# Kernel tuning notes

Hardware: AMD Instinct MI355X
Metric: run time of the kernel (lower is better)

Reference implementation:

```python
import math
import jax, jax.numpy as jnp
import numpy as np

D_MODEL = 512
N_HEADS = 8
D_K = D_MODEL // N_HEADS
LN_EPS = 1e-5


def _rel_pos_encoding(length: int, d: int) -> jnp.ndarray:
    """Sinusoidal encodings for positions 0..length-1, shape (length, d)."""
    pos = jnp.arange(length, dtype=jnp.float32)[:, None]            # (L,1)
    div = jnp.exp(jnp.arange(0, d, 2, dtype=jnp.float32) * (-(math.log(10000.0) / d)))  # (d/2,)
    ang = pos * div[None, :]                                         # (L,d/2)
    # interleave sin (even cols) and cos (odd cols)
    return jnp.stack([jnp.sin(ang), jnp.cos(ang)], axis=-1).reshape(length, d)


def setup_inputs() -> dict:
    key = jax.random.key(0)
    ks = jax.random.split(key, 6)
    B, T = 4, 2048
    s = 1.0 / math.sqrt(D_MODEL)
    return {
        "x":    jax.random.normal(ks[0], (B, T, D_MODEL), dtype=jnp.float32),
        "ln_g": jnp.ones((D_MODEL,), jnp.float32),
        "ln_b": jnp.zeros((D_MODEL,), jnp.float32),
        "wq":   jax.random.normal(ks[1], (D_MODEL, D_MODEL), jnp.float32) * s,
        "bq":   jnp.zeros((D_MODEL,), jnp.float32),
        "wk":   jax.random.normal(ks[2], (D_MODEL, D_MODEL), jnp.float32) * s,
        "bk":   jnp.zeros((D_MODEL,), jnp.float32),
        "wv":   jax.random.normal(ks[3], (D_MODEL, D_MODEL), jnp.float32) * s,
        "bv":   jnp.zeros((D_MODEL,), jnp.float32),
        "wo":   jax.random.normal(ks[4], (D_MODEL, D_MODEL), jnp.float32) * s,
        "bo":   jnp.zeros((D_MODEL,), jnp.float32),
    }


def reference(x, ln_g, ln_b, wq, bq, wk, bk, wv, bv, wo, bo):
    B, T, D = x.shape
    # pre-norm LayerNorm
    mu = jnp.mean(x, axis=-1, keepdims=True)
    var = jnp.mean(jnp.square(x - mu), axis=-1, keepdims=True)
    normed = (x - mu) * jax.lax.rsqrt(var + LN_EPS) * ln_g + ln_b

    def split_heads(y):  # (B,T,D) -> (B,H,T,dk)
        return y.reshape(B, T, N_HEADS, D_K).transpose(0, 2, 1, 3)

    Q = split_heads(normed @ wq.T + bq)
    K = split_heads(normed @ wk.T + bk)
    V = split_heads(normed @ wv.T + bv)

    pe = _rel_pos_encoding(T, D_K)            # (T, dk)
    K = K + pe[None, None, :, :]              # additive relative PE on K

    scale = 1.0 / math.sqrt(D_K)
    scores = jnp.einsum('bhtd,bhsd->bhts', Q, K) * scale   # (B,H,T,T)
    attn = jax.nn.softmax(scores, axis=-1)
    context = jnp.einsum('bhts,bhsd->bhtd', attn, V)        # (B,H,T,dk)
    context = context.transpose(0, 2, 1, 3).reshape(B, T, D)
    return context @ wo.T + bo
```

## Files before the change

### kernel.cpp

```cpp
#include <hip/hip_runtime.h>
#include <hip/hip_bf16.h>
#include <math.h>

#define D_MODEL 512
#define N_HEADS 8
#define D_K     64
#define T_SEQ   2048
#define B_SZ    4
#define M_ROWS  (B_SZ * T_SEQ)

typedef __bf16 bf16;
typedef __bf16 bf16x4 __attribute__((ext_vector_type(4)));
typedef __bf16 bf16x8 __attribute__((ext_vector_type(8)));
typedef float  floatx4 __attribute__((ext_vector_type(4)));

__device__ __forceinline__ int SWZ(int row, int col) {
  return row * 64 + ((((col >> 3) ^ (row & 7)) << 3) | (col & 7));
}

__device__ __forceinline__ float pe_fast(int t, int d) {
  int i2 = d & ~1;
  float div = __expf((float)i2 * (-0.1439115683f));
  float ang = (float)t * div;
  return (d & 1) ? __cosf(ang) : __sinf(ang);
}

__global__ __launch_bounds__(256) void prep(
    const float* __restrict__ x, const float* __restrict__ g,
    const float* __restrict__ b, bf16* __restrict__ out,
    const float* __restrict__ wq, const float* __restrict__ wk,
    const float* __restrict__ wv, const float* __restrict__ wo,
    bf16* __restrict__ wdst) {
  int bid = blockIdx.x;
  int tid = threadIdx.x;
  if (bid >= M_ROWS / 4) {
    int gid = (bid - M_ROWS / 4) * 256 + tid;
    int e0  = gid * 4;
    int mat = e0 >> 18;
    int loc = e0 & 262143;
    const float* src = (mat == 0) ? wq : (mat == 1) ? wk : (mat == 2) ? wv : wo;
    float4 v = *(const float4*)(src + loc);
    bf16x4 pk;
    pk[0] = (bf16)v.x; pk[1] = (bf16)v.y; pk[2] = (bf16)v.z; pk[3] = (bf16)v.w;
    *(bf16x4*)(wdst + e0) = pk;
    return;
  }
  int wave = tid >> 6, lane = tid & 63;
  int row  = bid * 4 + wave;
  const float* xr = x + (size_t)row * D_MODEL + lane * 8;
  float4 a = *(const float4*)(xr);
  float4 c = *(const float4*)(xr + 4);
  float s  = a.x + a.y + a.z + a.w + c.x + c.y + c.z + c.w;
  float ss = a.x * a.x + a.y * a.y + a.z * a.z + a.w * a.w +
             c.x * c.x + c.y * c.y + c.z * c.z + c.w * c.w;
#pragma unroll
  for (int off = 1; off < 64; off <<= 1) {
    s  += __shfl_xor(s,  off, 64);
    ss += __shfl_xor(ss, off, 64);
  }
  float mu  = s * (1.0f / D_MODEL);
  float var = ss * (1.0f / D_MODEL) - mu * mu;
  float rs  = rsqrtf(var + 1e-5f);
  float4 g0 = *(const float4*)(g + lane * 8);
  float4 g1 = *(const float4*)(g + lane * 8 + 4);
  float4 b0 = *(const float4*)(b + lane * 8);
  float4 b1 = *(const float4*)(b + lane * 8 + 4);
  bf16x8 o8;
  o8[0] = (bf16)((a.x - mu) * rs * g0.x + b0.x);
  o8[1] = (bf16)((a.y - mu) * rs * g0.y + b0.y);
  o8[2] = (bf16)((a.z - mu) * rs * g0.z + b0.z);
  o8[3] = (bf16)((a.w - mu) * rs * g0.w + b0.w);
  o8[4] = (bf16)((c.x - mu) * rs * g1.x + b1.x);
  o8[5] = (bf16)((c.y - mu) * rs * g1.y + b1.y);
  o8[6] = (bf16)((c.z - mu) * rs * g1.z + b1.z);
  o8[7] = (bf16)((c.w - mu) * rs * g1.w + b1.w);
  *(bf16x8*)(out + (size_t)row * D_MODEL + lane * 8) = o8;
}

__global__ __launch_bounds__(256, 3) void gemm_qkv(
    const bf16* __restrict__ A, const bf16* __restrict__ wqkv,
    const float* __restrict__ bq, const float* __restrict__ bk, const float* __restrict__ bv,
    bf16* __restrict__ Qo, bf16* __restrict__ Ko, bf16* __restrict__ VTo) {
  __shared__ bf16 sW[16384];
  __shared__ bf16 ep[4][1536];

  int tid = threadIdx.x;
  int w = tid >> 6, lane = tid & 63;
  int lm = lane & 15, quad = lane >> 4;
  int mat  = blockIdx.y >> 3;
  int h    = blockIdx.y & 7;
  int nloc = h * 64;
  const bf16* Wp = wqkv + (size_t)mat * 262144;

  int mbase = blockIdx.x * 128 + w * 32;
  const bf16* ap = A + (size_t)(mbase + lm) * D_MODEL + quad * 8;

  floatx4 acc[2][4];
#pragma unroll
  for (int mi = 0; mi < 2; mi++)
#pragma unroll
    for (int nt = 0; nt < 4; nt++) acc[mi][nt] = floatx4{0.f, 0.f, 0.f, 0.f};

  int srow = tid >> 2;
  int scc  = (tid & 3) * 16;

#pragma unroll 1
  for (int kp = 0; kp < 2; kp++) {
    if (kp) __syncthreads();
#pragma unroll
    for (int kc = 0; kc < 4; kc++) {
      const bf16* src = Wp + (size_t)(nloc + srow) * D_MODEL + kp * 256 + kc * 64 + scc;
      bf16x8 w0 = *(const bf16x8*)src;
      bf16x8 w1 = *(const bf16x8*)(src + 8);
      *(bf16x8*)&sW[kc * 4096 + SWZ(srow, scc)]     = w0;
      *(bf16x8*)&sW[kc * 4096 + SWZ(srow, scc + 8)] = w1;
    }
    __syncthreads();

    bf16x8 af[2][8];
#pragma unroll
    for (int mi = 0; mi < 2; mi++)
#pragma unroll
      for (int ks = 0; ks < 8; ks++)
        af[mi][ks] = *(const bf16x8*)(ap + mi * 16 * D_MODEL + kp * 256 + ks * 32);

#pragma unroll
    for (int ks = 0; ks < 8; ks++) {
#pragma unroll
      for (int nt = 0; nt < 4; nt++) {
        bf16x8 bfr = *(const bf16x8*)
            &sW[(ks >> 1) * 4096 + SWZ(nt * 16 + lm, (ks & 1) * 32 + quad * 8)];
        acc[0][nt] = __builtin_amdgcn_mfma_f32_16x16x32_bf16(af[0][ks], bfr, acc[0][nt], 0, 0, 0);
        acc[1][nt] = __builtin_amdgcn_mfma_f32_16x16x32_bf16(af[1][ks], bfr, acc[1][nt], 0, 0, 0);
      }
    }
  }

  int bb = mbase >> 11, t0w = mbase & (T_SEQ - 1);
  size_t bhoff = (size_t)(bb * N_HEADS + h) * (T_SEQ * D_K);
  bf16* myep = ep[w];

  if (mat == 2) {
#pragma unroll
    for (int nt = 0; nt < 4; nt++) {
      float bvv = bv[nloc + nt * 16 + lm];
#pragma unroll
      for (int mi = 0; mi < 2; mi++) {
        bf16x4 pk;
#pragma unroll
        for (int rr = 0; rr < 4; rr++) pk[rr] = (bf16)(acc[mi][nt][rr] + bvv);
        *(bf16x4*)&myep[lm * 40 + mi * 16 + quad * 4] = pk;
      }
      int dl = lane >> 2, toff = (lane & 3) * 8;
      bf16x8 v = *(const bf16x8*)&myep[dl * 40 + toff];
      *(bf16x8*)(VTo + bhoff + (size_t)(nt * 16 + dl) * T_SEQ + t0w + toff) = v;
    }
  } else {
    bf16* dst = (mat == 0) ? Qo : Ko;
    const float* bias = (mat == 0) ? bq : bk;
#pragma unroll
    for (int c = 0; c < 2; c++) {
#pragma unroll
      for (int nt = 0; nt < 4; nt++) {
        int d = nt * 16 + lm;
        float bval = bias[nloc + d];
#pragma unroll
        for (int rr = 0; rr < 4; rr++) {
          float v = acc[c][nt][rr] + bval;
          if (mat == 1) v += pe_fast(t0w + c * 16 + quad * 4 + rr, d);
          else          v *= 0.125f;
          myep[(quad * 4 + rr) * 72 + d] = (bf16)v;
        }
      }
#pragma unroll
      for (int rd = 0; rd < 2; rd++) {
        int row = rd * 8 + (lane >> 3);
        bf16x8 v = *(const bf16x8*)&myep[row * 72 + (lane & 7) * 8];
        *(bf16x8*)(dst + bhoff + (size_t)(t0w + c * 16 + row) * D_K + (lane & 7) * 8) = v;
      }
    }
  }
}

__global__ __launch_bounds__(256, 3) void gemm_out(const bf16* __restrict__ A,
                                                   const bf16* __restrict__ W,
                                                   const float* __restrict__ bias,
                                                   float* __restrict__ out) {
  __shared__ bf16 sW[16384];
  int tid = threadIdx.x;
  int w = tid >> 6, lane = tid & 63;
  int lm = lane & 15, quad = lane >> 4;
  int n0 = blockIdx.y * 64;

  int mbase = blockIdx.x * 128 + w * 32;
  const bf16* ap = A + (size_t)(mbase + lm) * D_MODEL + quad * 8;

  floatx4 acc[2][4];
#pragma unroll
  for (int mi = 0; mi < 2; mi++)
#pragma unroll
    for (int nt = 0; nt < 4; nt++) acc[mi][nt] = floatx4{0.f, 0.f, 0.f, 0.f};

  int srow = tid >> 2;
  int scc  = (tid & 3) * 16;

#pragma unroll 1
  for (int kp = 0; kp < 2; kp++) {
    if (kp) __syncthreads();
#pragma unroll
    for (int kc = 0; kc < 4; kc++) {
      const bf16* src = W + (size_t)(n0 + srow) * D_MODEL + kp * 256 + kc * 64 + scc;
      bf16x8 w0 = *(const bf16x8*)src;
      bf16x8 w1 = *(const bf16x8*)(src + 8);
      *(bf16x8*)&sW[kc * 4096 + SWZ(srow, scc)]     = w0;
      *(bf16x8*)&sW[kc * 4096 + SWZ(srow, scc + 8)] = w1;
    }
    __syncthreads();

    bf16x8 af[2][8];
#pragma unroll
    for (int mi = 0; mi < 2; mi++)
#pragma unroll
      for (int ks = 0; ks < 8; ks++)
        af[mi][ks] = *(const bf16x8*)(ap + mi * 16 * D_MODEL + kp * 256 + ks * 32);

#pragma unroll
    for (int ks = 0; ks < 8; ks++) {
#pragma unroll
      for (int nt = 0; nt < 4; nt++) {
        bf16x8 bfr = *(const bf16x8*)
            &sW[(ks >> 1) * 4096 + SWZ(nt * 16 + lm, (ks & 1) * 32 + quad * 8)];
        acc[0][nt] = __builtin_amdgcn_mfma_f32_16x16x32_bf16(af[0][ks], bfr, acc[0][nt], 0, 0, 0);
        acc[1][nt] = __builtin_amdgcn_mfma_f32_16x16x32_bf16(af[1][ks], bfr, acc[1][nt], 0, 0, 0);
      }
    }
  }

#pragma unroll
  for (int nt = 0; nt < 4; nt++) {
    int n = n0 + nt * 16 + lm;
    float bval = bias[n];
#pragma unroll
    for (int mi = 0; mi < 2; mi++)
#pragma unroll
      for (int rr = 0; rr < 4; rr++) {
        int m = mbase + mi * 16 + quad * 4 + rr;
        out[(size_t)m * D_MODEL + n] = acc[mi][nt][rr] + bval;
      }
  }
}

__global__ __launch_bounds__(512, 4) void flash_mfma(const bf16* __restrict__ Q,
                                                     const bf16* __restrict__ K,
                                                     const bf16* __restrict__ VT,
                                                     bf16* __restrict__ ctx) {
  __shared__ __align__(16) char smem[65536];
  bf16* sK  = (bf16*)smem;
  bf16* sVT = (bf16*)(smem + 16384);
  bf16* sP  = (bf16*)(smem + 32768);

  int tid  = threadIdx.x;
  int wave = tid >> 6, lane = tid & 63;
  int lm = lane & 15, quad = lane >> 4;
  int qg = wave & 3, kg = wave >> 2;
  int bh = blockIdx.y;
  int q0 = blockIdx.x * 128 + qg * 32;

  const bf16* Qb  = Q  + (size_t)bh * T_SEQ * D_K;
  const bf16* Kb  = K  + (size_t)bh * T_SEQ * D_K;
  const bf16* VTb = VT + (size_t)bh * T_SEQ * D_K;

  bf16x8 qf[2][2];
#pragma unroll
  for (int qt = 0; qt < 2; qt++)
#pragma unroll
    for (int kb = 0; kb < 2; kb++)
      qf[qt][kb] = *(const bf16x8*)(Qb + (size_t)(q0 + qt * 16 + lm) * D_K + kb * 32 + quad * 8);

  floatx4 o[2][4];
#pragma unroll
  for (int qt = 0; qt < 2; qt++)
#pragma unroll
    for (int nt = 0; nt < 4; nt++) o[qt][nt] = floatx4{0.f, 0.f, 0.f, 0.f};
  float l_i[2] = {0.f, 0.f};

  int srow = tid >> 3;
  int scol = (tid & 7) * 8;
  const bf16* kp0 = Kb  + (size_t)srow * D_K + scol;
  const bf16* vp0 = VTb + (size_t)srow * T_SEQ + scol;

  bf16x8 rk[2], rv[2];
  rk[0] = *(const bf16x8*)(kp0);
  rk[1] = *(const bf16x8*)(kp0 + 4096);
  rv[0] = *(const bf16x8*)(vp0);
  rv[1] = *(const bf16x8*)(vp0 + 64);

  bf16* myK = sK  + kg * 4096;
  bf16* myV = sVT + kg * 4096;
  bf16* myP = sP  + wave * 2048;

  for (int r = 0; r < T_SEQ / 64; r += 2) {
    __syncthreads();
    *(bf16x8*)&sK [SWZ(srow, scol)]         = rk[0];
    *(bf16x8*)&sK [4096 + SWZ(srow, scol)]  = rk[1];
    *(bf16x8*)&sVT[SWZ(srow, scol)]         = rv[0];
    *(bf16x8*)&sVT[4096 + SWZ(srow, scol)]  = rv[1];
    if (r + 2 < T_SEQ / 64) {
      rk[0] = *(const bf16x8*)(kp0 + (r + 2) * 4096);
      rk[1] = *(const bf16x8*)(kp0 + (r + 3) * 4096);
      rv[0] = *(const bf16x8*)(vp0 + (r + 2) * 64);
      rv[1] = *(const bf16x8*)(vp0 + (r + 3) * 64);
    }
    __syncthreads();

#pragma unroll
    for (int nt = 0; nt < 4; nt++) {
      floatx4 s0 = floatx4{0.f, 0.f, 0.f, 0.f};
      floatx4 s1 = floatx4{0.f, 0.f, 0.f, 0.f};
#pragma unroll
      for (int kb = 0; kb < 2; kb++) {
        bf16x8 kf = *(const bf16x8*)&myK[SWZ(nt * 16 + lm, kb * 32 + quad * 8)];
        s0 = __builtin_amdgcn_mfma_f32_16x16x32_bf16(kf, qf[0][kb], s0, 0, 0, 0);
        s1 = __builtin_amdgcn_mfma_f32_16x16x32_bf16(kf, qf[1][kb], s1, 0, 0, 0);
      }
      bf16x4 pk0, pk1;
#pragma unroll
      for (int rr = 0; rr < 4; rr++) {
        float p0 = __expf(s0[rr] - 8.0f);
        float p1 = __expf(s1[rr] - 8.0f);
        l_i[0] += p0; l_i[1] += p1;
        pk0[rr] = (bf16)p0; pk1[rr] = (bf16)p1;
      }
      *(bf16x4*)&myP[SWZ(lm,      nt * 16 + quad * 4)] = pk0;
      *(bf16x4*)&myP[SWZ(16 + lm, nt * 16 + quad * 4)] = pk1;
    }

#pragma unroll
    for (int kb = 0; kb < 2; kb++) {
      bf16x8 pf0 = *(const bf16x8*)&myP[SWZ(lm, kb * 32 + quad * 8)];
      bf16x8 pf1 = *(const bf16x8*)&myP[SWZ(16 + lm, kb * 32 + quad * 8)];
#pragma unroll
      for (int nt = 0; nt < 4; nt++) {
        bf16x8 vt = *(const bf16x8*)&myV[SWZ(nt * 16 + lm, kb * 32 + quad * 8)];
        o[0][nt] = __builtin_amdgcn_mfma_f32_16x16x32_bf16(pf0, vt, o[0][nt], 0, 0, 0);
        o[1][nt] = __builtin_amdgcn_mfma_f32_16x16x32_bf16(pf1, vt, o[1][nt], 0, 0, 0);
      }
    }
  }

#pragma unroll
  for (int qt = 0; qt < 2; qt++) {
    l_i[qt] += __shfl_xor(l_i[qt], 16, 64);
    l_i[qt] += __shfl_xor(l_i[qt], 32, 64);
  }

  __syncthreads();
  float* scO = (float*)smem;
  float* scL = (float*)(smem + 32768);
  if (kg == 1) {
#pragma unroll
    for (int qt = 0; qt < 2; qt++)
#pragma unroll
      for (int nt = 0; nt < 4; nt++)
        *(floatx4*)&scO[(qg * 512 + (qt * 4 + nt) * 64 + lane) * 4] = o[qt][nt];
    scL[qg * 128 + lane]      = l_i[0];
    scL[qg * 128 + 64 + lane] = l_i[1];
  }
  __syncthreads();
  if (kg == 0) {
#pragma unroll
    for (int qt = 0; qt < 2; qt++)
#pragma unroll
      for (int nt = 0; nt < 4; nt++) {
        floatx4 t = *(const floatx4*)&scO[(qg * 512 + (qt * 4 + nt) * 64 + lane) * 4];
        o[qt][nt] += t;
      }
    l_i[0] += scL[qg * 128 + lane];
    l_i[1] += scL[qg * 128 + 64 + lane];

    int b_ = bh >> 3, h = bh & 7;
#pragma unroll
    for (int qt = 0; qt < 2; qt++) {
#pragma unroll
      for (int rr = 0; rr < 4; rr++) {
        int qq = quad * 4 + rr;
        float linv = 1.f / __shfl(l_i[qt], qq, 64);
        int t = q0 + qt * 16 + qq;
        bf16* op = ctx + ((size_t)(b_ * T_SEQ + t)) * D_MODEL + h * D_K;
#pragma unroll
        for (int nt = 0; nt < 4; nt++)
          op[nt * 16 + lm] = (bf16)(o[qt][nt][rr] * linv);
      }
    }
  }
}

extern "C" void kernel_launch(void* const* d_in, const int* in_sizes, int n_in,
                              void* d_out, int out_size, void* d_ws, size_t ws_size,
                              hipStream_t stream) {
  const float* x    = (const float*)d_in[0];
  const float* ln_g = (const float*)d_in[1];
  const float* ln_b = (const float*)d_in[2];
  const float* wq   = (const float*)d_in[3];
  const float* bq   = (const float*)d_in[4];
  const float* wk   = (const float*)d_in[5];
  const float* bk   = (const float*)d_in[6];
  const float* wv   = (const float*)d_in[7];
  const float* bv   = (const float*)d_in[8];
  const float* wo   = (const float*)d_in[9];
  const float* bo   = (const float*)d_in[10];
  float* out = (float*)d_out;

  char* ws = (char*)d_ws;
  const size_t MB8 = (size_t)M_ROWS * D_MODEL * sizeof(bf16);
  bf16* normed = (bf16*)(ws);
  bf16* Qb     = (bf16*)(ws + MB8);
  bf16* Kb     = (bf16*)(ws + 2 * MB8);
  bf16* VTb    = (bf16*)(ws + 3 * MB8);
  bf16* w4     = (bf16*)(ws + 4 * MB8);
  bf16* ctx    = normed;

  prep<<<M_ROWS / 4 + 1024, 256, 0, stream>>>(x, ln_g, ln_b, normed,
                                              wq, wk, wv, wo, w4);
  gemm_qkv<<<dim3(64, 24), 256, 0, stream>>>(
      normed, w4, bq, bk, bv, Qb, Kb, VTb);
  flash_mfma<<<dim3(T_SEQ / 128, B_SZ * N_HEADS), 512, 0, stream>>>(Qb, Kb, VTb, ctx);
  gemm_out<<<dim3(64, 8), 256, 0, stream>>>(
      ctx, w4 + 3 * (size_t)D_MODEL * D_MODEL, bo, out);
}
```

Before: 177.1 us.

## Switch flash attention to 32x32x16 MFMA with register-resident P via permlane swap

Rewrites the attention inner loop to use 32x32x16 bf16 MFMA tiles instead of 16x16x32. The probability matrix is no longer staged through LDS: it is converted with v_cvt_pk_bf16_f32 and rearranged across lane halves with v_permlane32_swap, so it can be fed directly as the A operand of the PV MFMA. This removes the LDS round trip for P, shrinks shared memory from 64KB to 34KB (possibly raising occupancy), and changes the final reduction and output layout to match. The register-level lane shuffle depends on an exact layout match between the MFMA output and input formats, which is a correctness risk.

After: 178.5 us. Within noise of the previous version (+0.8%).

```diff
diff --git a/kernel.cpp b/kernel.cpp
--- a/kernel.cpp
+++ b/kernel.cpp
@@ -13,9 +13,20 @@
 typedef __bf16 bf16x4 __attribute__((ext_vector_type(4)));
 typedef __bf16 bf16x8 __attribute__((ext_vector_type(8)));
 typedef float  floatx4 __attribute__((ext_vector_type(4)));
+typedef float  floatx16 __attribute__((ext_vector_type(16)));
 
 __device__ __forceinline__ int SWZ(int row, int col) {
   return row * 64 + ((((col >> 3) ^ (row & 7)) << 3) | (col & 7));
+}
+
+__device__ __forceinline__ unsigned cvtpk(float a, float b) {
+  unsigned r;
+  asm volatile("v_cvt_pk_bf16_f32 %0, %1, %2" : "=v"(r) : "v"(a), "v"(b));
+  return r;
+}
+
+__device__ __forceinline__ void plswap(unsigned& a, unsigned& b) {
+  asm volatile("v_permlane32_swap_b32 %0, %1" : "+v"(a), "+v"(b));
 }
 
 __device__ __forceinline__ float pe_fast(int t, int d) {
@@ -254,14 +265,13 @@
                                                      const bf16* __restrict__ K,
                                                      const bf16* __restrict__ VT,
                                                      bf16* __restrict__ ctx) {
-  __shared__ __align__(16) char smem[65536];
+  __shared__ __align__(16) char smem[34816];
   bf16* sK  = (bf16*)smem;
   bf16* sVT = (bf16*)(smem + 16384);
-  bf16* sP  = (bf16*)(smem + 32768);
 
   int tid  = threadIdx.x;
   int wave = tid >> 6, lane = tid & 63;
-  int lm = lane & 15, quad = lane >> 4;
+  int lq = lane & 31, hi = lane >> 5;
   int qg = wave & 3, kg = wave >> 2;
   int bh = blockIdx.y;
   int q0 = blockIdx.x * 128 + qg * 32;
@@ -270,19 +280,15 @@
   const bf16* Kb  = K  + (size_t)bh * T_SEQ * D_K;
   const bf16* VTb = VT + (size_t)bh * T_SEQ * D_K;
 
-  bf16x8 qf[2][2];
-#pragma unroll
-  for (int qt = 0; qt < 2; qt++)
-#pragma unroll
-    for (int kb = 0; kb < 2; kb++)
-      qf[qt][kb] = *(const bf16x8*)(Qb + (size_t)(q0 + qt * 16 + lm) * D_K + kb * 32 + quad * 8);
-
-  floatx4 o[2][4];
-#pragma unroll
-  for (int qt = 0; qt < 2; qt++)
-#pragma unroll
-    for (int nt = 0; nt < 4; nt++) o[qt][nt] = floatx4{0.f, 0.f, 0.f, 0.f};
-  float l_i[2] = {0.f, 0.f};
+  bf16x8 qf[4];
+#pragma unroll
+  for (int c = 0; c < 4; c++)
+    qf[c] = *(const bf16x8*)(Qb + (size_t)(q0 + lq) * D_K + c * 16 + hi * 8);
+
+  floatx16 o0 = {0.f}, o1 = {0.f};
+#pragma unroll
+  for (int r = 0; r < 16; r++) { o0[r] = 0.f; o1[r] = 0.f; }
+  float l_i = 0.f;
 
   int srow = tid >> 3;
   int scol = (tid & 7) * 8;
@@ -297,7 +303,6 @@
 
   bf16* myK = sK  + kg * 4096;
   bf16* myV = sVT + kg * 4096;
-  bf16* myP = sP  + wave * 2048;
 
   for (int r = 0; r < T_SEQ / 64; r += 2) {
     __syncthreads();
@@ -314,83 +319,71 @@
     __syncthreads();
 
 #pragma unroll
-    for (int nt = 0; nt < 4; nt++) {
-      floatx4 s0 = floatx4{0.f, 0.f, 0.f, 0.f};
-      floatx4 s1 = floatx4{0.f, 0.f, 0.f, 0.f};
-#pragma unroll
-      for (int kb = 0; kb < 2; kb++) {
-        bf16x8 kf = *(const bf16x8*)&myK[SWZ(nt * 16 + lm, kb * 32 + quad * 8)];
-        s0 = __builtin_amdgcn_mfma_f32_16x16x32_bf16(kf, qf[0][kb], s0, 0, 0, 0);
-        s1 = __builtin_amdgcn_mfma_f32_16x16x32_bf16(kf, qf[1][kb], s1, 0, 0, 0);
-      }
-      bf16x4 pk0, pk1;
-#pragma unroll
-      for (int rr = 0; rr < 4; rr++) {
-        float p0 = __expf(s0[rr] - 8.0f);
-        float p1 = __expf(s1[rr] - 8.0f);
-        l_i[0] += p0; l_i[1] += p1;
-        pk0[rr] = (bf16)p0; pk1[rr] = (bf16)p1;
-      }
-      *(bf16x4*)&myP[SWZ(lm,      nt * 16 + quad * 4)] = pk0;
-      *(bf16x4*)&myP[SWZ(16 + lm, nt * 16 + quad * 4)] = pk1;
-    }
-
-#pragma unroll
-    for (int kb = 0; kb < 2; kb++) {
-      bf16x8 pf0 = *(const bf16x8*)&myP[SWZ(lm, kb * 32 + quad * 8)];
-      bf16x8 pf1 = *(const bf16x8*)&myP[SWZ(16 + lm, kb * 32 + quad * 8)];
-#pragma unroll
-      for (int nt = 0; nt < 4; nt++) {
-        bf16x8 vt = *(const bf16x8*)&myV[SWZ(nt * 16 + lm, kb * 32 + quad * 8)];
-        o[0][nt] = __builtin_amdgcn_mfma_f32_16x16x32_bf16(pf0, vt, o[0][nt], 0, 0, 0);
-        o[1][nt] = __builtin_amdgcn_mfma_f32_16x16x32_bf16(pf1, vt, o[1][nt], 0, 0, 0);
-      }
-    }
-  }
-
-#pragma unroll
-  for (int qt = 0; qt < 2; qt++) {
-    l_i[qt] += __shfl_xor(l_i[qt], 16, 64);
-    l_i[qt] += __shfl_xor(l_i[qt], 32, 64);
-  }
+    for (int sub = 0; sub < 2; sub++) {
+      floatx16 s;
+#pragma unroll
+      for (int rr = 0; rr < 16; rr++) s[rr] = 0.f;
+#pragma unroll
+      for (int c = 0; c < 4; c++) {
+        bf16x8 kf = *(const bf16x8*)&myK[SWZ(sub * 32 + lq, c * 16 + hi * 8)];
+        s = __builtin_amdgcn_mfma_f32_32x32x16_bf16(kf, qf[c], s, 0, 0, 0);
+      }
+      float p[16];
+#pragma unroll
+      for (int rr = 0; rr < 16; rr++) {
+        p[rr] = __expf(s[rr] - 8.0f);
+        l_i += p[rr];
+      }
+#pragma unroll
+      for (int kc = 0; kc < 2; kc++) {
+        unsigned w0 = cvtpk(p[kc * 8 + 0], p[kc * 8 + 1]);
+        unsigned w1 = cvtpk(p[kc * 8 + 2], p[kc * 8 + 3]);
+        unsigned w2 = cvtpk(p[kc * 8 + 4], p[kc * 8 + 5]);
+        unsigned w3 = cvtpk(p[kc * 8 + 6], p[kc * 8 + 7]);
+        plswap(w0, w2);
+        plswap(w1, w3);
+        union { unsigned u[4]; bf16x8 v; } pu;
+        pu.u[0] = w0; pu.u[1] = w1; pu.u[2] = w2; pu.u[3] = w3;
+        int kcol = sub * 32 + kc * 16 + hi * 8;
+        bf16x8 vb0 = *(const bf16x8*)&myV[SWZ(lq,      kcol)];
+        bf16x8 vb1 = *(const bf16x8*)&myV[SWZ(32 + lq, kcol)];
+        o0 = __builtin_amdgcn_mfma_f32_32x32x16_bf16(pu.v, vb0, o0, 0, 0, 0);
+        o1 = __builtin_amdgcn_mfma_f32_32x32x16_bf16(pu.v, vb1, o1, 0, 0, 0);
+      }
+    }
+  }
+
+  l_i += __shfl_xor(l_i, 32, 64);
 
   __syncthreads();
   float* scO = (float*)smem;
   float* scL = (float*)(smem + 32768);
   if (kg == 1) {
 #pragma unroll
-    for (int qt = 0; qt < 2; qt++)
-#pragma unroll
-      for (int nt = 0; nt < 4; nt++)
-        *(floatx4*)&scO[(qg * 512 + (qt * 4 + nt) * 64 + lane) * 4] = o[qt][nt];
-    scL[qg * 128 + lane]      = l_i[0];
-    scL[qg * 128 + 64 + lane] = l_i[1];
+    for (int rr = 0; rr < 16; rr++) {
+      scO[((qg * 2 + 0) * 16 + rr) * 64 + lane] = o0[rr];
+      scO[((qg * 2 + 1) * 16 + rr) * 64 + lane] = o1[rr];
+    }
+    if (lane < 32) scL[qg * 32 + lq] = l_i;
   }
   __syncthreads();
   if (kg == 0) {
 #pragma unroll
-    for (int qt = 0; qt < 2; qt++)
-#pragma unroll
-      for (int nt = 0; nt < 4; nt++) {
-        floatx4 t = *(const floatx4*)&scO[(qg * 512 + (qt * 4 + nt) * 64 + lane) * 4];
-        o[qt][nt] += t;
-      }
-    l_i[0] += scL[qg * 128 + lane];
-    l_i[1] += scL[qg * 128 + 64 + lane];
+    for (int rr = 0; rr < 16; rr++) {
+      o0[rr] += scO[((qg * 2 + 0) * 16 + rr) * 64 + lane];
+      o1[rr] += scO[((qg * 2 + 1) * 16 + rr) * 64 + lane];
+    }
+    l_i += scL[qg * 32 + lq];
 
     int b_ = bh >> 3, h = bh & 7;
 #pragma unroll
-    for (int qt = 0; qt < 2; qt++) {
-#pragma unroll
-      for (int rr = 0; rr < 4; rr++) {
-        int qq = quad * 4 + rr;
-        float linv = 1.f / __shfl(l_i[qt], qq, 64);
-        int t = q0 + qt * 16 + qq;
-        bf16* op = ctx + ((size_t)(b_ * T_SEQ + t)) * D_MODEL + h * D_K;
-#pragma unroll
-        for (int nt = 0; nt < 4; nt++)
-          op[nt * 16 + lm] = (bf16)(o[qt][nt][rr] * linv);
-      }
+    for (int rr = 0; rr < 16; rr++) {
+      int qq = (rr & 3) + 8 * (rr >> 2) + 4 * hi;
+      float linv = 1.f / __shfl(l_i, qq, 64);
+      int t = q0 + qq;
+      bf16* op = ctx + ((size_t)(b_ * T_SEQ + t)) * D_MODEL + h * D_K + lq;
+      op[0]  = (bf16)(o0[rr] * linv);
+      op[32] = (bf16)(o1[rr] * linv);
     }
   }
 }
```
